# Performance work log

Hardware: AMD Instinct MI355X
Metric: run time of the kernel (lower is better)

## Reference

```python
import jax, jax.numpy as jnp
import numpy as np

N, E, D, H, G = 50000, 640000, 128, 128, 64
EPS = 1e-5


def gcn_conv(x, row, col, W, b, n):
    # PyG GCNConv: linear transform, symmetric deg^-1/2 normalization (self-loops
    # already appended to row/col), scatter-add aggregation, then bias.
    h = x @ W  # [N, H]
    ones = jnp.ones(row.shape[0], dtype=h.dtype)
    deg = jax.ops.segment_sum(ones, col, num_segments=n)
    dinv = jnp.where(deg > 0, jax.lax.rsqrt(deg), 0.0)
    norm = dinv[row] * dinv[col]                       # [E+N]
    msg = h[row] * norm[:, None]                       # gather + scale
    out = jax.ops.segment_sum(msg, col, num_segments=n)  # scatter-add
    return out + b


def graph_layernorm(x, w, b):
    # PyG LayerNorm(mode='graph') with batch=None: normalize over the whole tensor.
    mu = x.mean()
    xc = x - mu
    std = jnp.sqrt((xc * xc).mean())
    return xc / (std + EPS) * w + b


def setup_inputs() -> dict:
    key = jax.random.key(0)
    ks = jax.random.split(key, 12)
    x = jax.random.normal(ks[0], (N, D), dtype=jnp.float32)
    edge_index = jax.random.randint(ks[1], (2, E), 0, N, dtype=jnp.int64)
    batch = jnp.sort(jax.random.randint(ks[2], (N,), 0, G, dtype=jnp.int64))
    s1 = 1.0 / np.sqrt(D)
    s2 = 1.0 / np.sqrt(H)
    return {
        "x": x,
        "edge_index": edge_index,
        "batch": batch,
        "W1": jax.random.normal(ks[3], (D, H), dtype=jnp.float32) * s1,
        "b1": jnp.zeros((H,), dtype=jnp.float32),
        "ln1_w": jnp.ones((H,), dtype=jnp.float32),
        "ln1_b": jnp.zeros((H,), dtype=jnp.float32),
        "W2": jax.random.normal(ks[4], (H, H), dtype=jnp.float32) * s2,
        "b2": jnp.zeros((H,), dtype=jnp.float32),
        "ln2_w": jnp.ones((H,), dtype=jnp.float32),
        "ln2_b": jnp.zeros((H,), dtype=jnp.float32),
        "fc_w": jax.random.normal(ks[5], (H, 1), dtype=jnp.float32) * s2,
        "fc_b": jnp.zeros((1,), dtype=jnp.float32),
    }


def reference(x, edge_index, batch, W1, b1, ln1_w, ln1_b, W2, b2, ln2_w, ln2_b, fc_w, fc_b):
    n = x.shape[0]
    loops = jnp.arange(n, dtype=edge_index.dtype)
    row = jnp.concatenate([edge_index[0], loops])  # add self-loops
    col = jnp.concatenate([edge_index[1], loops])

    h = gcn_conv(x, row, col, W1, b1, n)
    h = jax.nn.relu(graph_layernorm(h, ln1_w, ln1_b))
    h = gcn_conv(h, row, col, W2, b2, n)
    h = jax.nn.relu(graph_layernorm(h, ln2_w, ln2_b))

    # global_mean_pool over batch segment ids
    sums = jax.ops.segment_sum(h, batch, num_segments=G)          # [G, H]
    cnt = jax.ops.segment_sum(jnp.ones((n,), h.dtype), batch, num_segments=G)
    pooled = sums / jnp.maximum(cnt, 1.0)[:, None]

    logits = pooled @ fc_w + fc_b                                  # [G, 1]
    return jax.nn.sigmoid(logits).squeeze(-1)                      # [G]
```

## Files before the change

### kernel.cpp

```cpp
#include <hip/hip_runtime.h>
#include <math.h>

#define H 128
#define PC 8

typedef _Float16 half8v __attribute__((ext_vector_type(8)));
typedef float floatx4 __attribute__((ext_vector_type(4)));

__device__ __forceinline__ int lower_bound_i(const int* a, int n, int key) {
  int lo = 0, hi = n;
  while (lo < hi) { int mid = (lo + hi) >> 1; if (a[mid] < key) lo = mid + 1; else hi = mid; }
  return lo;
}

__global__ void k_initpack(const float* __restrict__ W1, const float* __restrict__ W2,
                           _Float16* __restrict__ PW1, _Float16* __restrict__ PW2,
                           int* cntE, int* cursor, float* slots, int n) {
  int b = blockIdx.x;
  int tid = threadIdx.x;
  if (b < 128) {
    int t = b * 256 + tid;
    const float* W = (t < 16384) ? W1 : W2;
    _Float16* PW = (t < 16384) ? PW1 : PW2;
    int u = t & 16383;
    int j = u & 7;
    int nn = (u >> 3) & 15;
    int quad = (u >> 7) & 3;
    int ks = (u >> 9) & 3;
    int ct = (u >> 11) & 7;
    PW[u] = (_Float16)W[(ks * 32 + quad * 8 + j) * H + ct * 16 + nn];
  } else {
    int i = (b - 128) * 256 + tid;
    int stride = 128 * 256;
    for (int j = i; j < n; j += stride) { cntE[j] = 0; cursor[j] = 0; }
    for (int j = i; j < 256; j += stride) slots[j] = 0.f;
  }
}

__global__ void k_count(const int* __restrict__ col, int* __restrict__ cntE, int E) {
  int e = blockIdx.x * blockDim.x + threadIdx.x;
  if (e < E) atomicAdd(&cntE[col[e]], 1);
}

__global__ void k_scan_block(const int* __restrict__ cnt, int* __restrict__ offs,
                             int* __restrict__ bsum, int n) {
  __shared__ int s[256];
  int tid = threadIdx.x;
  int i = blockIdx.x * 256 + tid;
  int v = (i < n) ? cnt[i] : 0;
  s[tid] = v;
  __syncthreads();
  for (int d = 1; d < 256; d <<= 1) {
    int t = (tid >= d) ? s[tid - d] : 0;
    __syncthreads();
    s[tid] += t;
    __syncthreads();
  }
  if (i < n) offs[i] = s[tid] - v;
  if (tid == 255) bsum[blockIdx.x] = s[255];
}

__global__ void k_scan_add(int* __restrict__ offs, const int* __restrict__ bsum,
                           const int* __restrict__ cntE, float* __restrict__ dinv, int n) {
  __shared__ int sh[4];
  int tid = threadIdx.x;
  int v = (tid < blockIdx.x) ? bsum[tid] : 0;
#pragma unroll
  for (int o = 32; o > 0; o >>= 1) v += __shfl_xor(v, o, 64);
  if ((tid & 63) == 0) sh[tid >> 6] = v;
  __syncthreads();
  int boff = sh[0] + sh[1] + sh[2] + sh[3];
  int i = blockIdx.x * 256 + tid;
  if (i < n) {
    offs[i] += boff;
    dinv[i] = rsqrtf((float)(cntE[i] + 1));
  }
}

__global__ void k_scatter(const int* __restrict__ row, const int* __restrict__ col,
                          const int* __restrict__ offs, int* __restrict__ cursor,
                          int* __restrict__ esrc, int E) {
  int e = blockIdx.x * blockDim.x + threadIdx.x;
  if (e < E) {
    int c = col[e];
    int p = atomicAdd(&cursor[c], 1);
    esrc[offs[c] + p] = row[e];
  }
}

__global__ __launch_bounds__(256) void k_gemm_mfma(const float* __restrict__ Xf,
                                                   const _Float16* __restrict__ Xh,
                                                   const _Float16* __restrict__ PW,
                                                   _Float16* __restrict__ O,
                                                   const float* __restrict__ lnw,
                                                   const float* __restrict__ lnb,
                                                   const float* __restrict__ slot,
                                                   float invM, int n) {
  int wave = blockIdx.x * 4 + (threadIdx.x >> 6);
  int tiles = (n + 15) >> 4;
  if (wave >= tiles) return;
  int lane = threadIdx.x & 63;
  int m = lane & 15;
  int quad = lane >> 4;
  int r0 = wave * 16;
  int row = r0 + m;
  if (row >= n) row = n - 1;

  bool ln = (slot != nullptr);
  float mu = 0.f, rs = 0.f;
  if (ln) {
    float s = slot[lane], q = slot[64 + lane];
#pragma unroll
    for (int o = 32; o > 0; o >>= 1) { s += __shfl_xor(s, o, 64); q += __shfl_xor(q, o, 64); }
    mu = s * invM;
    float var = fmaxf(q * invM - mu * mu, 0.f);
    rs = 1.f / (sqrtf(var) + 1e-5f);
  }

  floatx4 acc[8] = {};
  const half8v* PB8 = (const half8v*)PW;

#pragma unroll
  for (int ks = 0; ks < 4; ks++) {
    int kb = ks * 32 + quad * 8;
    half8v a;
    if (Xf) {
      const float* xr = Xf + (size_t)row * H + kb;
      float4 u0 = *(const float4*)xr;
      float4 u1 = *(const float4*)(xr + 4);
      a[0] = (_Float16)u0.x; a[1] = (_Float16)u0.y; a[2] = (_Float16)u0.z; a[3] = (_Float16)u0.w;
      a[4] = (_Float16)u1.x; a[5] = (_Float16)u1.y; a[6] = (_Float16)u1.z; a[7] = (_Float16)u1.w;
    } else {
      half8v hv = *(const half8v*)(Xh + (size_t)row * H + kb);
      if (ln) {
        float4 w0 = *(const float4*)(lnw + kb);
        float4 w1 = *(const float4*)(lnw + kb + 4);
        float4 c0 = *(const float4*)(lnb + kb);
        float4 c1 = *(const float4*)(lnb + kb + 4);
        a[0] = (_Float16)fmaxf(((float)hv[0] - mu) * rs * w0.x + c0.x, 0.f);
        a[1] = (_Float16)fmaxf(((float)hv[1] - mu) * rs * w0.y + c0.y, 0.f);
        a[2] = (_Float16)fmaxf(((float)hv[2] - mu) * rs * w0.z + c0.z, 0.f);
        a[3] = (_Float16)fmaxf(((float)hv[3] - mu) * rs * w0.w + c0.w, 0.f);
        a[4] = (_Float16)fmaxf(((float)hv[4] - mu) * rs * w1.x + c1.x, 0.f);
        a[5] = (_Float16)fmaxf(((float)hv[5] - mu) * rs * w1.y + c1.y, 0.f);
        a[6] = (_Float16)fmaxf(((float)hv[6] - mu) * rs * w1.z + c1.z, 0.f);
        a[7] = (_Float16)fmaxf(((float)hv[7] - mu) * rs * w1.w + c1.w, 0.f);
      } else {
        a = hv;
      }
    }
#pragma unroll
    for (int ct = 0; ct < 8; ct++) {
      half8v b = PB8[((ct * 4 + ks) * 4 + quad) * 16 + m];
      acc[ct] = __builtin_amdgcn_mfma_f32_16x16x32_f16(a, b, acc[ct], 0, 0, 0);
    }
  }

#pragma unroll
  for (int ct = 0; ct < 8; ct++) {
#pragma unroll
    for (int reg = 0; reg < 4; reg++) {
      int ro = r0 + quad * 4 + reg;
      if (ro < n) O[(size_t)ro * H + ct * 16 + m] = (_Float16)acc[ct][reg];
    }
  }
}

__global__ __launch_bounds__(256) void k_agg(const _Float16* __restrict__ Hs,
                                             _Float16* __restrict__ Out,
                                             const int* __restrict__ esrc, const int* __restrict__ offs,
                                             const int* __restrict__ cntE, const float* __restrict__ dinv,
                                             const float* __restrict__ bias, float* __restrict__ slot,
                                             int n) {
  int sub = threadIdx.x >> 4;
  int lane = threadIdx.x & 15;
  int i = blockIdx.x * 16 + sub;
  float sv = 0.f, sq = 0.f;
  if (i < n) {
    float di = dinv[i];
    half8v hself = *(const half8v*)&Hs[(size_t)i * H + 8 * lane];
    float acc[8];
#pragma unroll
    for (int e = 0; e < 8; e++) acc[e] = di * (float)hself[e];
    int beg = offs[i], cnt = cntE[i];
    for (int base = 0; base < cnt; base += 16) {
      int mm = cnt - base; if (mm > 16) mm = 16;
      int sid = 0; float dv = 0.f;
      if (lane < mm) { sid = esrc[beg + base + lane]; dv = dinv[sid]; }
      int j = 0;
      for (; j + 8 <= mm; j += 8) {
        int sg[8]; float dg[8]; half8v hg[8];
#pragma unroll
        for (int u = 0; u < 8; u++) {
          sg[u] = __shfl(sid, j + u, 16);
          dg[u] = __shfl(dv, j + u, 16);
        }
#pragma unroll
        for (int u = 0; u < 8; u++) hg[u] = *(const half8v*)&Hs[(size_t)sg[u] * H + 8 * lane];
#pragma unroll
        for (int e = 0; e < 8; e++) {
          float t = 0.f;
#pragma unroll
          for (int u = 0; u < 8; u++) t += dg[u] * (float)hg[u][e];
          acc[e] += t;
        }
      }
      for (; j + 4 <= mm; j += 4) {
        int s0 = __shfl(sid, j + 0, 16);
        int s1 = __shfl(sid, j + 1, 16);
        int s2 = __shfl(sid, j + 2, 16);
        int s3 = __shfl(sid, j + 3, 16);
        float d0 = __shfl(dv, j + 0, 16);
        float d1 = __shfl(dv, j + 1, 16);
        float d2 = __shfl(dv, j + 2, 16);
        float d3 = __shfl(dv, j + 3, 16);
        half8v h0 = *(const half8v*)&Hs[(size_t)s0 * H + 8 * lane];
        half8v h1 = *(const half8v*)&Hs[(size_t)s1 * H + 8 * lane];
        half8v h2 = *(const half8v*)&Hs[(size_t)s2 * H + 8 * lane];
        half8v h3 = *(const half8v*)&Hs[(size_t)s3 * H + 8 * lane];
#pragma unroll
        for (int e = 0; e < 8; e++)
          acc[e] += d0 * (float)h0[e] + d1 * (float)h1[e] + d2 * (float)h2[e] + d3 * (float)h3[e];
      }
      for (; j < mm; j++) {
        int s = __shfl(sid, j, 16);
        float d = __shfl(dv, j, 16);
        half8v hv = *(const half8v*)&Hs[(size_t)s * H + 8 * lane];
#pragma unroll
        for (int e = 0; e < 8; e++) acc[e] += d * (float)hv[e];
      }
    }
    const float* bb = bias + 8 * lane;
    half8v vo;
#pragma unroll
    for (int e = 0; e < 8; e++) {
      float v = di * acc[e] + bb[e];
      vo[e] = (_Float16)v;
      sv += v;
      sq += v * v;
    }
    *(half8v*)&Out[(size_t)i * H + 8 * lane] = vo;
  }
#pragma unroll
  for (int o = 32; o > 0; o >>= 1) {
    sv += __shfl_xor(sv, o, 64);
    sq += __shfl_xor(sq, o, 64);
  }
  __shared__ float rsm[4], rqm[4];
  int wave = threadIdx.x >> 6;
  if ((threadIdx.x & 63) == 0) { rsm[wave] = sv; rqm[wave] = sq; }
  __syncthreads();
  if (threadIdx.x == 0) {
    float ts = rsm[0] + rsm[1] + rsm[2] + rsm[3];
    float tq = rqm[0] + rqm[1] + rqm[2] + rqm[3];
    int sl = blockIdx.x & 63;
    atomicAdd(&slot[sl], ts);
    atomicAdd(&slot[64 + sl], tq);
  }
}

__global__ __launch_bounds__(128) void k_pool(const _Float16* __restrict__ Hs,
                                              const int* __restrict__ batch,
                                              const float* __restrict__ lnw, const float* __restrict__ lnb,
                                              const float* __restrict__ slot, float invM,
                                              float* __restrict__ psum, int n) {
  int g = blockIdx.x / PC, q = blockIdx.x % PC;
  int t = threadIdx.x;
  int l = t & 63;
  float s = slot[l], qq = slot[64 + l];
#pragma unroll
  for (int o = 32; o > 0; o >>= 1) { s += __shfl_xor(s, o, 64); qq += __shfl_xor(qq, o, 64); }
  float mu = s * invM;
  float var = fmaxf(qq * invM - mu * mu, 0.f);
  float rs = 1.f / (sqrtf(var) + 1e-5f);

  int start = lower_bound_i(batch, n, g);
  int end = lower_bound_i(batch, n, g + 1);
  int tot = end - start;
  int per = (tot + PC - 1) / PC;
  int s0 = start + q * per;
  int e0 = s0 + per; if (e0 > end) e0 = end;
  float w = lnw[t], bb = lnb[t];
  float acc = 0.f;
  for (int i = s0; i < e0; i++) {
    float v = (float)Hs[(size_t)i * H + t];
    v = (v - mu) * rs * w + bb;
    acc += fmaxf(v, 0.f);
  }
  psum[(size_t)blockIdx.x * H + t] = acc;
}

__global__ __launch_bounds__(128) void k_fc(const float* __restrict__ psum, const int* __restrict__ batch,
                                            const float* __restrict__ fcw, const float* __restrict__ fcb,
                                            float* __restrict__ out, int n) {
  int g = blockIdx.x;
  int t = threadIdx.x;
  int start = lower_bound_i(batch, n, g);
  int end = lower_bound_i(batch, n, g + 1);
  float cnt = fmaxf((float)(end - start), 1.f);
  float tot = 0.f;
#pragma unroll
  for (int c = 0; c < PC; c++) tot += psum[(size_t)(g * PC + c) * H + t];
  float v = tot / cnt * fcw[t];
  int lane = t & 63, wave = t >> 6;
#pragma unroll
  for (int o = 32; o > 0; o >>= 1) v += __shfl_xor(v, o, 64);
  __shared__ float r2[2];
  if (lane == 0) r2[wave] = v;
  __syncthreads();
  if (t == 0) {
    float logit = r2[0] + r2[1] + fcb[0];
    out[g] = 1.f / (1.f + expf(-logit));
  }
}

extern "C" void kernel_launch(void* const* d_in, const int* in_sizes, int n_in,
                              void* d_out, int out_size, void* d_ws, size_t ws_size,
                              hipStream_t stream) {
  const float* x    = (const float*)d_in[0];
  const int*   ei   = (const int*)d_in[1];
  const int*   batch= (const int*)d_in[2];
  const float* W1   = (const float*)d_in[3];
  const float* b1   = (const float*)d_in[4];
  const float* ln1w = (const float*)d_in[5];
  const float* ln1b = (const float*)d_in[6];
  const float* W2   = (const float*)d_in[7];
  const float* b2   = (const float*)d_in[8];
  const float* ln2w = (const float*)d_in[9];
  const float* ln2b = (const float*)d_in[10];
  const float* fcw  = (const float*)d_in[11];
  const float* fcb  = (const float*)d_in[12];
  float* out = (float*)d_out;

  int N = in_sizes[2];
  int E = in_sizes[1] / 2;
  int G = out_size;

  char* p = (char*)d_ws;
  int*   cntE   = (int*)p;   p += (size_t)N * 4;
  int*   offs   = (int*)p;   p += (size_t)N * 4;
  int*   cursor = (int*)p;   p += (size_t)N * 4;
  float* dinv   = (float*)p; p += (size_t)N * 4;
  int*   esrc   = (int*)p;   p += (size_t)E * 4;
  _Float16* bufA = (_Float16*)p; p += (size_t)N * H * 2;
  _Float16* bufB = (_Float16*)p; p += (size_t)N * H * 2;
  _Float16* PW1  = (_Float16*)p; p += 16384 * 2;
  _Float16* PW2  = (_Float16*)p; p += 16384 * 2;
  float* slots  = (float*)p; p += 256 * 4;
  int*   bsum   = (int*)p;   p += 256 * 4;
  float* psum   = (float*)p; p += (size_t)G * PC * H * 4;

  const int* row = ei;
  const int* col = ei + E;

  k_initpack<<<256, 256, 0, stream>>>(W1, W2, PW1, PW2, cntE, cursor, slots, N);
  k_count<<<(E + 255) / 256, 256, 0, stream>>>(col, cntE, E);
  int NB = (N + 255) / 256;
  k_scan_block<<<NB, 256, 0, stream>>>(cntE, offs, bsum, N);
  k_scan_add<<<NB, 256, 0, stream>>>(offs, bsum, cntE, dinv, N);
  k_scatter<<<(E + 255) / 256, 256, 0, stream>>>(row, col, offs, cursor, esrc, E);

  int tiles = (N + 15) / 16;
  int GB = (tiles + 3) / 4;
  float invM = 1.f / ((float)N * (float)H);

  k_gemm_mfma<<<GB, 256, 0, stream>>>(x, nullptr, PW1, bufA, nullptr, nullptr, nullptr, 0.f, N);
  k_agg<<<(N + 15) / 16, 256, 0, stream>>>(bufA, bufB, esrc, offs, cntE, dinv, b1, slots, N);
  k_gemm_mfma<<<GB, 256, 0, stream>>>(nullptr, bufB, PW2, bufA, ln1w, ln1b, slots, invM, N);
  k_agg<<<(N + 15) / 16, 256, 0, stream>>>(bufA, bufB, esrc, offs, cntE, dinv, b2, slots + 128, N);
  k_pool<<<G * PC, 128, 0, stream>>>(bufB, batch, ln2w, ln2b, slots + 128, invM, psum, N);
  k_fc<<<G, 128, 0, stream>>>(psum, batch, fcw, fcb, out, N);
}
```

Baseline: 299.1 us.

## Prescale GEMM output by dinv, record edge slots at count, fuse scatter into GEMM1

The count kernel now keeps the atomic return value as each edge's slot within its destination. This removes the second atomic pass and the cursor buffer. The scatter of source ids runs in the same launch as the first GEMM, using a block-index split. Both GEMMs multiply their output rows by dinv of the source node, so aggregation only sums gathered rows and no longer gathers and shuffles per-edge dinv values. The cost is an extra E-sized perm buffer, and fp16 rounding now happens after scaling.

```diff
diff --git a/kernel.cpp b/kernel.cpp
--- a/kernel.cpp
+++ b/kernel.cpp
@@ -15,7 +15,7 @@
 
 __global__ void k_initpack(const float* __restrict__ W1, const float* __restrict__ W2,
                            _Float16* __restrict__ PW1, _Float16* __restrict__ PW2,
-                           int* cntE, int* cursor, float* slots, int n) {
+                           int* cntE, float* slots, int n) {
   int b = blockIdx.x;
   int tid = threadIdx.x;
   if (b < 128) {
@@ -32,14 +32,15 @@
   } else {
     int i = (b - 128) * 256 + tid;
     int stride = 128 * 256;
-    for (int j = i; j < n; j += stride) { cntE[j] = 0; cursor[j] = 0; }
+    for (int j = i; j < n; j += stride) cntE[j] = 0;
     for (int j = i; j < 256; j += stride) slots[j] = 0.f;
   }
 }
 
-__global__ void k_count(const int* __restrict__ col, int* __restrict__ cntE, int E) {
+__global__ void k_count(const int* __restrict__ col, int* __restrict__ cntE,
+                        int* __restrict__ perm, int E) {
   int e = blockIdx.x * blockDim.x + threadIdx.x;
-  if (e < E) atomicAdd(&cntE[col[e]], 1);
+  if (e < E) perm[e] = atomicAdd(&cntE[col[e]], 1);
 }
 
 __global__ void k_scan_block(const int* __restrict__ cnt, int* __restrict__ offs,
@@ -77,25 +78,78 @@
   }
 }
 
-__global__ void k_scatter(const int* __restrict__ row, const int* __restrict__ col,
-                          const int* __restrict__ offs, int* __restrict__ cursor,
-                          int* __restrict__ esrc, int E) {
-  int e = blockIdx.x * blockDim.x + threadIdx.x;
-  if (e < E) {
-    int c = col[e];
-    int p = atomicAdd(&cursor[c], 1);
-    esrc[offs[c] + p] = row[e];
-  }
-}
-
-__global__ __launch_bounds__(256) void k_gemm_mfma(const float* __restrict__ Xf,
-                                                   const _Float16* __restrict__ Xh,
-                                                   const _Float16* __restrict__ PW,
-                                                   _Float16* __restrict__ O,
-                                                   const float* __restrict__ lnw,
-                                                   const float* __restrict__ lnb,
-                                                   const float* __restrict__ slot,
-                                                   float invM, int n) {
+__device__ __forceinline__ void gemm_tile_f32(const float* __restrict__ Xf,
+                                              const _Float16* __restrict__ PW,
+                                              const float* __restrict__ dinv,
+                                              _Float16* __restrict__ O,
+                                              int wave, int laneid, int n) {
+  int m = laneid & 15;
+  int quad = laneid >> 4;
+  int r0 = wave * 16;
+  int row = r0 + m;
+  if (row >= n) row = n - 1;
+  floatx4 acc[8] = {};
+  const half8v* PB8 = (const half8v*)PW;
+#pragma unroll
+  for (int ks = 0; ks < 4; ks++) {
+    int kb = ks * 32 + quad * 8;
+    const float* xr = Xf + (size_t)row * H + kb;
+    float4 u0 = *(const float4*)xr;
+    float4 u1 = *(const float4*)(xr + 4);
+    half8v a;
+    a[0] = (_Float16)u0.x; a[1] = (_Float16)u0.y; a[2] = (_Float16)u0.z; a[3] = (_Float16)u0.w;
+    a[4] = (_Float16)u1.x; a[5] = (_Float16)u1.y; a[6] = (_Float16)u1.z; a[7] = (_Float16)u1.w;
+#pragma unroll
+    for (int ct = 0; ct < 8; ct++) {
+      half8v b = PB8[((ct * 4 + ks) * 4 + quad) * 16 + m];
+      acc[ct] = __builtin_amdgcn_mfma_f32_16x16x32_f16(a, b, acc[ct], 0, 0, 0);
+    }
+  }
+  float dv[4];
+#pragma unroll
+  for (int reg = 0; reg < 4; reg++) {
+    int ro = r0 + quad * 4 + reg;
+    dv[reg] = (ro < n) ? dinv[ro] : 0.f;
+  }
+#pragma unroll
+  for (int ct = 0; ct < 8; ct++) {
+#pragma unroll
+    for (int reg = 0; reg < 4; reg++) {
+      int ro = r0 + quad * 4 + reg;
+      if (ro < n) O[(size_t)ro * H + ct * 16 + m] = (_Float16)(acc[ct][reg] * dv[reg]);
+    }
+  }
+}
+
+__global__ __launch_bounds__(256) void k_sg1(const int* __restrict__ row, const int* __restrict__ col,
+                                             const int* __restrict__ offs, const int* __restrict__ perm,
+                                             int* __restrict__ esrc, int E,
+                                             const float* __restrict__ Xf,
+                                             const _Float16* __restrict__ PW,
+                                             const float* __restrict__ dinv,
+                                             _Float16* __restrict__ O, int n, int GB) {
+  int b = blockIdx.x;
+  if (b < GB) {
+    int wave = b * 4 + (threadIdx.x >> 6);
+    int tiles = (n + 15) >> 4;
+    if (wave >= tiles) return;
+    gemm_tile_f32(Xf, PW, dinv, O, wave, threadIdx.x & 63, n);
+  } else {
+    int e = (b - GB) * 256 + threadIdx.x;
+    if (e < E) {
+      int c = col[e];
+      esrc[offs[c] + perm[e]] = row[e];
+    }
+  }
+}
+
+__global__ __launch_bounds__(256) void k_gemm2(const _Float16* __restrict__ Xh,
+                                               const _Float16* __restrict__ PW,
+                                               const float* __restrict__ lnw,
+                                               const float* __restrict__ lnb,
+                                               const float* __restrict__ slot, float invM,
+                                               const float* __restrict__ dinv,
+                                               _Float16* __restrict__ O, int n) {
   int wave = blockIdx.x * 4 + (threadIdx.x >> 6);
   int tiles = (n + 15) >> 4;
   if (wave >= tiles) return;
@@ -106,67 +160,55 @@
   int row = r0 + m;
   if (row >= n) row = n - 1;
 
-  bool ln = (slot != nullptr);
-  float mu = 0.f, rs = 0.f;
-  if (ln) {
-    float s = slot[lane], q = slot[64 + lane];
-#pragma unroll
-    for (int o = 32; o > 0; o >>= 1) { s += __shfl_xor(s, o, 64); q += __shfl_xor(q, o, 64); }
-    mu = s * invM;
-    float var = fmaxf(q * invM - mu * mu, 0.f);
-    rs = 1.f / (sqrtf(var) + 1e-5f);
-  }
+  float s = slot[lane], q = slot[64 + lane];
+#pragma unroll
+  for (int o = 32; o > 0; o >>= 1) { s += __shfl_xor(s, o, 64); q += __shfl_xor(q, o, 64); }
+  float mu = s * invM;
+  float var = fmaxf(q * invM - mu * mu, 0.f);
+  float rs = 1.f / (sqrtf(var) + 1e-5f);
 
   floatx4 acc[8] = {};
   const half8v* PB8 = (const half8v*)PW;
-
 #pragma unroll
   for (int ks = 0; ks < 4; ks++) {
     int kb = ks * 32 + quad * 8;
+    half8v hv = *(const half8v*)(Xh + (size_t)row * H + kb);
+    float4 w0 = *(const float4*)(lnw + kb);
+    float4 w1 = *(const float4*)(lnw + kb + 4);
+    float4 c0 = *(const float4*)(lnb + kb);
+    float4 c1 = *(const float4*)(lnb + kb + 4);
     half8v a;
-    if (Xf) {
-      const float* xr = Xf + (size_t)row * H + kb;
-      float4 u0 = *(const float4*)xr;
-      float4 u1 = *(const float4*)(xr + 4);
-      a[0] = (_Float16)u0.x; a[1] = (_Float16)u0.y; a[2] = (_Float16)u0.z; a[3] = (_Float16)u0.w;
-      a[4] = (_Float16)u1.x; a[5] = (_Float16)u1.y; a[6] = (_Float16)u1.z; a[7] = (_Float16)u1.w;
-    } else {
-      half8v hv = *(const half8v*)(Xh + (size_t)row * H + kb);
-      if (ln) {
-        float4 w0 = *(const float4*)(lnw + kb);
-        float4 w1 = *(const float4*)(lnw + kb + 4);
-        float4 c0 = *(const float4*)(lnb + kb);
-        float4 c1 = *(const float4*)(lnb + kb + 4);
-        a[0] = (_Float16)fmaxf(((float)hv[0] - mu) * rs * w0.x + c0.x, 0.f);
-        a[1] = (_Float16)fmaxf(((float)hv[1] - mu) * rs * w0.y + c0.y, 0.f);
-        a[2] = (_Float16)fmaxf(((float)hv[2] - mu) * rs * w0.z + c0.z, 0.f);
-        a[3] = (_Float16)fmaxf(((float)hv[3] - mu) * rs * w0.w + c0.w, 0.f);
-        a[4] = (_Float16)fmaxf(((float)hv[4] - mu) * rs * w1.x + c1.x, 0.f);
-        a[5] = (_Float16)fmaxf(((float)hv[5] - mu) * rs * w1.y + c1.y, 0.f);
-        a[6] = (_Float16)fmaxf(((float)hv[6] - mu) * rs * w1.z + c1.z, 0.f);
-        a[7] = (_Float16)fmaxf(((float)hv[7] - mu) * rs * w1.w + c1.w, 0.f);
-      } else {
-        a = hv;
-      }
-    }
+    a[0] = (_Float16)fmaxf(((float)hv[0] - mu) * rs * w0.x + c0.x, 0.f);
+    a[1] = (_Float16)fmaxf(((float)hv[1] - mu) * rs * w0.y + c0.y, 0.f);
+    a[2] = (_Float16)fmaxf(((float)hv[2] - mu) * rs * w0.z + c0.z, 0.f);
+    a[3] = (_Float16)fmaxf(((float)hv[3] - mu) * rs * w0.w + c0.w, 0.f);
+    a[4] = (_Float16)fmaxf(((float)hv[4] - mu) * rs * w1.x + c1.x, 0.f);
+    a[5] = (_Float16)fmaxf(((float)hv[5] - mu) * rs * w1.y + c1.y, 0.f);
+    a[6] = (_Float16)fmaxf(((float)hv[6] - mu) * rs * w1.z + c1.z, 0.f);
+    a[7] = (_Float16)fmaxf(((float)hv[7] - mu) * rs * w1.w + c1.w, 0.f);
 #pragma unroll
     for (int ct = 0; ct < 8; ct++) {
       half8v b = PB8[((ct * 4 + ks) * 4 + quad) * 16 + m];
       acc[ct] = __builtin_amdgcn_mfma_f32_16x16x32_f16(a, b, acc[ct], 0, 0, 0);
     }
   }
-
+  float dv[4];
+#pragma unroll
+  for (int reg = 0; reg < 4; reg++) {
+    int ro = r0 + quad * 4 + reg;
+    dv[reg] = (ro < n) ? dinv[ro] : 0.f;
+  }
 #pragma unroll
   for (int ct = 0; ct < 8; ct++) {
 #pragma unroll
     for (int reg = 0; reg < 4; reg++) {
       int ro = r0 + quad * 4 + reg;
-      if (ro < n) O[(size_t)ro * H + ct * 16 + m] = (_Float16)acc[ct][reg];
-    }
-  }
-}
-
-__global__ __launch_bounds__(256) void k_agg(const _Float16* __restrict__ Hs,
+      if (ro < n) O[(size_t)ro * H + ct * 16 + m] = (_Float16)(acc[ct][reg] * dv[reg]);
+    }
+  }
+}
+
+__global__ __launch_bounds__(256) void k_agg(const _Float16* __restrict__ Gs,
                                              _Float16* __restrict__ Out,
                                              const int* __restrict__ esrc, const int* __restrict__ offs,
                                              const int* __restrict__ cntE, const float* __restrict__ dinv,
@@ -178,30 +220,27 @@
   float sv = 0.f, sq = 0.f;
   if (i < n) {
     float di = dinv[i];
-    half8v hself = *(const half8v*)&Hs[(size_t)i * H + 8 * lane];
+    half8v gself = *(const half8v*)&Gs[(size_t)i * H + 8 * lane];
     float acc[8];
 #pragma unroll
-    for (int e = 0; e < 8; e++) acc[e] = di * (float)hself[e];
+    for (int e = 0; e < 8; e++) acc[e] = (float)gself[e];
     int beg = offs[i], cnt = cntE[i];
     for (int base = 0; base < cnt; base += 16) {
       int mm = cnt - base; if (mm > 16) mm = 16;
-      int sid = 0; float dv = 0.f;
-      if (lane < mm) { sid = esrc[beg + base + lane]; dv = dinv[sid]; }
+      int sid = 0;
+      if (lane < mm) sid = esrc[beg + base + lane];
       int j = 0;
       for (; j + 8 <= mm; j += 8) {
-        int sg[8]; float dg[8]; half8v hg[8];
-#pragma unroll
-        for (int u = 0; u < 8; u++) {
-          sg[u] = __shfl(sid, j + u, 16);
-          dg[u] = __shfl(dv, j + u, 16);
-        }
-#pragma unroll
-        for (int u = 0; u < 8; u++) hg[u] = *(const half8v*)&Hs[(size_t)sg[u] * H + 8 * lane];
+        int sg[8]; half8v hg[8];
+#pragma unroll
+        for (int u = 0; u < 8; u++) sg[u] = __shfl(sid, j + u, 16);
+#pragma unroll
+        for (int u = 0; u < 8; u++) hg[u] = *(const half8v*)&Gs[(size_t)sg[u] * H + 8 * lane];
 #pragma unroll
         for (int e = 0; e < 8; e++) {
           float t = 0.f;
 #pragma unroll
-          for (int u = 0; u < 8; u++) t += dg[u] * (float)hg[u][e];
+          for (int u = 0; u < 8; u++) t += (float)hg[u][e];
           acc[e] += t;
         }
       }
@@ -210,24 +249,19 @@
         int s1 = __shfl(sid, j + 1, 16);
         int s2 = __shfl(sid, j + 2, 16);
         int s3 = __shfl(sid, j + 3, 16);
-        float d0 = __shfl(dv, j + 0, 16);
-        float d1 = __shfl(dv, j + 1, 16);
-        float d2 = __shfl(dv, j + 2, 16);
-        float d3 = __shfl(dv, j + 3, 16);
-        half8v h0 = *(const half8v*)&Hs[(size_t)s0 * H + 8 * lane];
-        half8v h1 = *(const half8v*)&Hs[(size_t)s1 * H + 8 * lane];
-        half8v h2 = *(const half8v*)&Hs[(size_t)s2 * H + 8 * lane];
-        half8v h3 = *(const half8v*)&Hs[(size_t)s3 * H + 8 * lane];
+        half8v h0 = *(const half8v*)&Gs[(size_t)s0 * H + 8 * lane];
+        half8v h1 = *(const half8v*)&Gs[(size_t)s1 * H + 8 * lane];
+        half8v h2 = *(const half8v*)&Gs[(size_t)s2 * H + 8 * lane];
+        half8v h3 = *(const half8v*)&Gs[(size_t)s3 * H + 8 * lane];
 #pragma unroll
         for (int e = 0; e < 8; e++)
-          acc[e] += d0 * (float)h0[e] + d1 * (float)h1[e] + d2 * (float)h2[e] + d3 * (float)h3[e];
+          acc[e] += (float)h0[e] + (float)h1[e] + (float)h2[e] + (float)h3[e];
       }
       for (; j < mm; j++) {
         int s = __shfl(sid, j, 16);
-        float d = __shfl(dv, j, 16);
-        half8v hv = *(const half8v*)&Hs[(size_t)s * H + 8 * lane];
-#pragma unroll
-        for (int e = 0; e < 8; e++) acc[e] += d * (float)hv[e];
+        half8v hv = *(const half8v*)&Gs[(size_t)s * H + 8 * lane];
+#pragma unroll
+        for (int e = 0; e < 8; e++) acc[e] += (float)hv[e];
       }
     }
     const float* bb = bias + 8 * lane;
@@ -339,8 +373,8 @@
   char* p = (char*)d_ws;
   int*   cntE   = (int*)p;   p += (size_t)N * 4;
   int*   offs   = (int*)p;   p += (size_t)N * 4;
-  int*   cursor = (int*)p;   p += (size_t)N * 4;
   float* dinv   = (float*)p; p += (size_t)N * 4;
+  int*   perm   = (int*)p;   p += (size_t)E * 4;
   int*   esrc   = (int*)p;   p += (size_t)E * 4;
   _Float16* bufA = (_Float16*)p; p += (size_t)N * H * 2;
   _Float16* bufB = (_Float16*)p; p += (size_t)N * H * 2;
@@ -353,20 +387,20 @@
   const int* row = ei;
   const int* col = ei + E;
 
-  k_initpack<<<256, 256, 0, stream>>>(W1, W2, PW1, PW2, cntE, cursor, slots, N);
-  k_count<<<(E + 255) / 256, 256, 0, stream>>>(col, cntE, E);
+  k_initpack<<<256, 256, 0, stream>>>(W1, W2, PW1, PW2, cntE, slots, N);
+  int EB = (E + 255) / 256;
+  k_count<<<EB, 256, 0, stream>>>(col, cntE, perm, E);
   int NB = (N + 255) / 256;
   k_scan_block<<<NB, 256, 0, stream>>>(cntE, offs, bsum, N);
   k_scan_add<<<NB, 256, 0, stream>>>(offs, bsum, cntE, dinv, N);
-  k_scatter<<<(E + 255) / 256, 256, 0, stream>>>(row, col, offs, cursor, esrc, E);
 
   int tiles = (N + 15) / 16;
   int GB = (tiles + 3) / 4;
   float invM = 1.f / ((float)N * (float)H);
 
-  k_gemm_mfma<<<GB, 256, 0, stream>>>(x, nullptr, PW1, bufA, nullptr, nullptr, nullptr, 0.f, N);
+  k_sg1<<<GB + EB, 256, 0, stream>>>(row, col, offs, perm, esrc, E, x, PW1, dinv, bufA, N, GB);
   k_agg<<<(N + 15) / 16, 256, 0, stream>>>(bufA, bufB, esrc, offs, cntE, dinv, b1, slots, N);
-  k_gemm_mfma<<<GB, 256, 0, stream>>>(nullptr, bufB, PW2, bufA, ln1w, ln1b, slots, invM, N);
+  k_gemm2<<<GB, 256, 0, stream>>>(bufB, PW2, ln1w, ln1b, slots, invM, dinv, bufA, N);
   k_agg<<<(N + 15) / 16, 256, 0, stream>>>(bufA, bufB, esrc, offs, cntE, dinv, b2, slots + 128, N);
   k_pool<<<G * PC, 128, 0, stream>>>(bufB, batch, ln2w, ln2b, slots + 128, invM, psum, N);
   k_fc<<<G, 128, 0, stream>>>(psum, batch, fcw, fcb, out, N);
```

Result: faster. 282.9 us (-5.4%).
